# Kernel optimization log

Measured on AMD Instinct MI355X. Metric: run time of the kernel, lower is better.

Reference implementation:

```python
import jax, jax.numpy as jnp
import numpy as np

HEADS = 4
DIM_HEAD = 32
SCALE = 10.0  # scale=10 init arg
HIDDEN = HEADS * DIM_HEAD


def _l2norm(t, eps=1e-12):
    # matches torch F.normalize(t, dim=-1): normalize over last axis (flattened spatial)
    n = jnp.sqrt(jnp.sum(t * t, axis=-1, keepdims=True))
    return t / jnp.maximum(n, eps)


def setup_inputs() -> dict:
    key = jax.random.key(0)
    k1, k2, k3, k4, k5 = jax.random.split(key, 5)
    b, dim, H, W = 2, 128, 64, 64
    x = jax.random.normal(k1, (b, dim, H, W), jnp.float32)
    y = jax.random.normal(k2, (b, dim, H, W), jnp.float32)
    # to_qkv: Conv2d(dim, 3*hidden, 1, bias=False) -> weight (3*hidden, dim)
    w_qkv = jax.random.normal(k3, (3 * HIDDEN, dim), jnp.float32) / np.sqrt(dim)
    # to_out: Conv2d(hidden, dim, 1) -> weight (dim, hidden) + bias (dim,)
    w_out = jax.random.normal(k4, (dim, HIDDEN), jnp.float32) / np.sqrt(HIDDEN)
    b_out = jax.random.normal(k5, (dim,), jnp.float32) * 0.01
    return {"x": x, "y": y, "w_qkv": w_qkv, "w_out": w_out, "b_out": b_out}


def reference(x, y, w_qkv, w_out, b_out):
    b, c, H, W = x.shape
    n_x = H * W
    n_y = y.shape[2] * y.shape[3]
    xf = x.reshape(b, c, n_x)
    yf = y.reshape(b, c, n_y)
    # 1x1 conv == channel GEMM
    qkv_x = jnp.einsum('oc,bcn->bon', w_qkv, xf)
    qkv_y = jnp.einsum('oc,bcn->bon', w_qkv, yf)
    # only q from x, k/v from y are used downstream
    q_x = qkv_x[:, :HIDDEN].reshape(b, HEADS, DIM_HEAD, n_x)
    k_y = qkv_y[:, HIDDEN:2 * HIDDEN].reshape(b, HEADS, DIM_HEAD, n_y)
    v_y = qkv_y[:, 2 * HIDDEN:].reshape(b, HEADS, DIM_HEAD, n_y)
    q = _l2norm(q_x)
    k = _l2norm(k_y)
    sim = jnp.einsum('bhdi,bhdj->bhij', q, k) * SCALE  # [b,h,n_x,n_y]
    attn = jax.nn.softmax(sim, axis=-1)
    out = jnp.einsum('bhij,bhdj->bhdi', attn, v_y)  # [b,h,d,n_x]
    out = out.reshape(b, HIDDEN, H, W)  # 'b h (x y) d -> b (h d) x y'
    return jnp.einsum('oc,bcHW->boHW', w_out, out) + b_out[None, :, None, None]
```

## Files before the change

kernel.cpp:

```cpp
#include <hip/hip_runtime.h>
#include <hip/hip_bf16.h>

#define HEADS 4
#define DIMH  32
#define HID   128
#define DIM   128
#define NSP   4096
#define QSCALE_LOG2E 14.426950408889634f

typedef __attribute__((ext_vector_type(4)))  float f32x4;
typedef __attribute__((ext_vector_type(16))) float f32x16;
typedef __attribute__((ext_vector_type(8)))  short s16x8;

__device__ __forceinline__ unsigned cvtpk_bf16(float a, float b) {
  unsigned d;
  asm("v_cvt_pk_bf16_f32 %0, %1, %2" : "=v"(d) : "v"(a), "v"(b));
  return d;
}

__global__ __launch_bounds__(256) void k_cvt(const float* __restrict__ x,
                                             const float* __restrict__ y,
                                             __hip_bfloat16* __restrict__ xt,
                                             __hip_bfloat16* __restrict__ yt) {
  int bid = blockIdx.x;
  int t = bid >> 7, rem = bid & 127;
  int b = rem >> 6, nt = rem & 63;
  int n0 = nt * 64;
  const float* src = (t ? y : x) + (size_t)b * DIM * NSP;
  __hip_bfloat16* dst = (t ? yt : xt) + (size_t)b * NSP * DIM;

  __shared__ alignas(16) __hip_bfloat16 tile[64 * 136];
  int n = threadIdx.x & 63, c0 = threadIdx.x >> 6;
  const float* sp = src + n0 + n;
#pragma unroll
  for (int cc = 0; cc < 32; ++cc) {
    int c = cc * 4 + c0;
    tile[n * 136 + c] = __float2bfloat16(sp[(size_t)c * NSP]);
  }
  __syncthreads();
  int rrow = threadIdx.x >> 2, cb = (threadIdx.x & 3) * 32;
  __hip_bfloat16* op = dst + (size_t)(n0 + rrow) * DIM + cb;
  const __hip_bfloat16* ip = tile + rrow * 136 + cb;
#pragma unroll
  for (int k = 0; k < 4; ++k)
    *(s16x8*)(op + k * 8) = *(const s16x8*)(ip + k * 8);
}

__global__ __launch_bounds__(256, 4) void k_qkvm(const __hip_bfloat16* __restrict__ xt,
                                                 const __hip_bfloat16* __restrict__ yt,
                                                 const float* __restrict__ w,
                                                 float* __restrict__ ssp,
                                                 float* __restrict__ Qf,
                                                 __hip_bfloat16* __restrict__ Kr,
                                                 __hip_bfloat16* __restrict__ Vb) {
  int xcd = blockIdx.x & 7;
  int r = blockIdx.x >> 3;
  int ot = r >> 2;
  int nts = r & 3;
  int tile = xcd * 4 + nts;
  int n0 = tile * 256;
  int lane = threadIdx.x & 63, wave = threadIdx.x >> 6;
  int l31 = lane & 31, hi = lane >> 5;
  int orow = ot * 32 + l31;

  s16x8 wf[8];
  const float* wr = w + orow * DIM + hi * 8;
#pragma unroll
  for (int k = 0; k < 8; ++k) {
    f32x4 a = *(const f32x4*)(wr + k * 16);
    f32x4 b2 = *(const f32x4*)(wr + k * 16 + 4);
    union { unsigned u[4]; s16x8 v; } p;
    p.u[0] = cvtpk_bf16(a[0], a[1]);
    p.u[1] = cvtpk_bf16(a[2], a[3]);
    p.u[2] = cvtpk_bf16(b2[0], b2[1]);
    p.u[3] = cvtpk_bf16(b2[2], b2[3]);
    wf[k] = p.v;
  }

  const __hip_bfloat16* src = (ot < 4 ? xt : yt);
  int nw = n0 + wave * 64;
  f32x16 acc0 = {}, acc1 = {};
#pragma unroll
  for (int k = 0; k < 8; ++k) {
    s16x8 b0 = *(const s16x8*)(src + (size_t)(nw + l31) * DIM + k * 16 + hi * 8);
    s16x8 b1 = *(const s16x8*)(src + (size_t)(nw + 32 + l31) * DIM + k * 16 + hi * 8);
    acc0 = __builtin_amdgcn_mfma_f32_32x32x16_bf16(wf[k], b0, acc0, 0, 0, 0);
    acc1 = __builtin_amdgcn_mfma_f32_32x32x16_bf16(wf[k], b1, acc1, 0, 0, 0);
  }

  int b = nw >> 12;
  if (ot < 8) {
    int h = ot & 3;
    if (ot < 4) {
#pragma unroll
      for (int nt = 0; nt < 2; ++nt) {
        int np = (nw + nt * 32 + l31) & 4095;
        float* base = Qf + ((size_t)((b * HEADS + h) * NSP + np)) * DIMH;
        const f32x16& A = nt ? acc1 : acc0;
#pragma unroll
        for (int m = 0; m < 4; ++m) {
          f32x4 v = { A[4 * m], A[4 * m + 1], A[4 * m + 2], A[4 * m + 3] };
          *(f32x4*)(base + 8 * m + 4 * hi) = v;
        }
      }
    } else {
#pragma unroll
      for (int nt = 0; nt < 2; ++nt) {
        int np = (nw + nt * 32 + l31) & 4095;
        __hip_bfloat16* base = Kr + ((size_t)((b * HEADS + h) * NSP + np)) * DIMH;
        const f32x16& A = nt ? acc1 : acc0;
#pragma unroll
        for (int m = 0; m < 4; ++m) {
          uint2 p2;
          p2.x = cvtpk_bf16(A[4 * m], A[4 * m + 1]);
          p2.y = cvtpk_bf16(A[4 * m + 2], A[4 * m + 3]);
          *(uint2*)(base + 8 * m + 4 * hi) = p2;
        }
      }
    }
    float p[16];
#pragma unroll
    for (int r2 = 0; r2 < 16; ++r2) p[r2] = acc0[r2] * acc0[r2] + acc1[r2] * acc1[r2];
#pragma unroll
    for (int r2 = 0; r2 < 16; ++r2) {
#pragma unroll
      for (int m2 = 1; m2 < 32; m2 <<= 1) p[r2] += __shfl_xor(p[r2], m2);
    }
    if (l31 == 0) {
      int t = (ot < 4 ? 0 : 1);
      int widx = (tile & 15) * 4 + wave;
      int rbase = (t * 2 + b) * 128 + h * 32;
#pragma unroll
      for (int r2 = 0; r2 < 16; ++r2) {
        int row = (r2 & 3) + 8 * (r2 >> 2) + 4 * hi;
        ssp[(size_t)(rbase + row) * 64 + widx] = p[r2];
      }
    }
  } else {
    int h = ot - 8;
#pragma unroll
    for (int nt = 0; nt < 2; ++nt) {
      int np = (nw + nt * 32 + l31) & 4095;
      const f32x16& A = nt ? acc1 : acc0;
#pragma unroll
      for (int r2 = 0; r2 < 16; ++r2) {
        int d = (r2 & 3) + 8 * (r2 >> 2) + 4 * hi;
        Vb[((size_t)((b * HEADS + h) * DIMH + d)) * NSP + np] = __float2bfloat16(A[r2]);
      }
    }
  }
}

__global__ __launch_bounds__(512) void k_fac(const float* __restrict__ ssp,
                                             float* __restrict__ fsc) {
  int bh = blockIdx.x;
  int b = bh >> 2, h = bh & 3;
  int tid = threadIdx.x;
  int qk = tid >> 8, d = (tid >> 3) & 31, jj = tid & 7;
  const float* pp = ssp + (size_t)((qk * 2 + b) * 128 + h * 32 + d) * 64 + jj * 8;
  float s = 0.f;
#pragma unroll
  for (int k = 0; k < 8; ++k) s += pp[k];
  s += __shfl_down(s, 1); s += __shfl_down(s, 2); s += __shfl_down(s, 4);
  __shared__ float red[2][32];
  if (jj == 0) red[qk][d] = s;
  __syncthreads();
  if (tid < 32) {
    float vq = 1.f / fmaxf(sqrtf(red[0][tid]), 0.1f);
    float vk = 1.f / fmaxf(sqrtf(red[1][tid]), 0.1f);
    fsc[bh * 32 + tid] = vq * vk * QSCALE_LOG2E;
  }
}

__device__ __forceinline__ void glds16(const __hip_bfloat16* g, __hip_bfloat16* l) {
  __builtin_amdgcn_global_load_lds(
      (const __attribute__((address_space(1))) unsigned int*)(const void*)g,
      (__attribute__((address_space(3))) unsigned int*)(void*)l, 16, 0, 0);
}

__device__ __forceinline__ void attn_sub2(const __hip_bfloat16* kbase,
                                          const __hip_bfloat16* vbase,
                                          int s, int l31, int hi,
                                          s16x8 qb0, s16x8 qb1,
                                          f32x16& O, float& lsum) {
  int krx = (l31 + (l31 >> 2)) & 3;
  int vrx = l31 & 7;
  const __hip_bfloat16* krow = kbase + (s * 32 + l31) * DIMH;
  s16x8 kf0 = *(const s16x8*)(krow + (((hi) ^ krx) << 3));
  s16x8 kf1 = *(const s16x8*)(krow + (((2 + hi) ^ krx) << 3));
  f32x16 z = {};
  f32x16 sv = __builtin_amdgcn_mfma_f32_32x32x16_bf16(kf0, qb0, z, 0, 0, 0);
  sv        = __builtin_amdgcn_mfma_f32_32x32x16_bf16(kf1, qb1, sv, 0, 0, 0);
  float p[16];
#pragma unroll
  for (int r = 0; r < 16; ++r) p[r] = __builtin_amdgcn_exp2f(sv[r]);
  float t0 = 0.f, t1 = 0.f;
#pragma unroll
  for (int r = 0; r < 16; r += 2) { t0 += p[r]; t1 += p[r + 1]; }
  lsum += t0 + t1;
  unsigned wA[4], wB[4];
#pragma unroll
  for (int m = 0; m < 4; ++m) {
    wA[m] = cvtpk_bf16(p[4 * m], p[4 * m + 1]);
    wB[m] = cvtpk_bf16(p[4 * m + 2], p[4 * m + 3]);
  }
  const __hip_bfloat16* vrow = vbase + l31 * 64;
#define PV_CHUNK(c2, vfrag)                                                    \
  {                                                                            \
    unsigned a0 = wA[2 * (c2)], a1 = wA[2 * (c2) + 1];                         \
    unsigned b0 = wB[2 * (c2)], b1 = wB[2 * (c2) + 1];                         \
    asm("v_permlane32_swap_b32 %0, %1" : "+v"(a0), "+v"(a1));                  \
    asm("v_permlane32_swap_b32 %0, %1" : "+v"(b0), "+v"(b1));                  \
    union { unsigned u[4]; s16x8 v; } pa;                                      \
    pa.u[0] = a0; pa.u[1] = b0; pa.u[2] = a1; pa.u[3] = b1;                    \
    O = __builtin_amdgcn_mfma_f32_32x32x16_bf16(pa.v, vfrag, O, 0, 0, 0);      \
  }
#pragma unroll
  for (int c2 = 0; c2 < 2; ++c2) {
    int cc = s * 2 + c2;
    s16x8 vf = *(const s16x8*)(vrow + (((cc * 2 + hi) ^ vrx) << 3));
    PV_CHUNK(c2, vf);
  }
#undef PV_CHUNK
}

__global__ __launch_bounds__(1024, 4) void k_attn(const float* __restrict__ Qf,
                                                  const __hip_bfloat16* __restrict__ Kt,
                                                  const __hip_bfloat16* __restrict__ Vb,
                                                  const float* __restrict__ fsc,
                                                  __hip_bfloat16* __restrict__ Otb) {
  int bh = blockIdx.x & 7, qt = blockIdx.x >> 3;
  int tid = threadIdx.x, lane = tid & 63, wave = tid >> 6;
  int qsub = wave & 3, jq = wave >> 2;
  int l31 = lane & 31, hi = lane >> 5;
  int i0 = qt * 128 + qsub * 32;
  int jbase = jq * 1024;

  __shared__ alignas(16) char smem[65536];
  __shared__ float Llds[16][64];
  __hip_bfloat16* KsB = (__hip_bfloat16*)smem;
  __hip_bfloat16* VsB = KsB + 16384;
  float* Olds = (float*)smem;

  const __hip_bfloat16* kg = Kt + (size_t)bh * NSP * DIMH;
  const __hip_bfloat16* vg = Vb + (size_t)bh * DIMH * NSP;

  const float* qpf = Qf + ((size_t)bh * NSP + i0 + l31) * DIMH;
  const float* fb = fsc + bh * 32;
  s16x8 qb0, qb1;
  {
    f32x4 a0 = *(const f32x4*)(qpf + hi * 8);
    f32x4 a1 = *(const f32x4*)(qpf + hi * 8 + 4);
    f32x4 a2 = *(const f32x4*)(qpf + 16 + hi * 8);
    f32x4 a3 = *(const f32x4*)(qpf + 16 + hi * 8 + 4);
    f32x4 f0 = *(const f32x4*)(fb + hi * 8);
    f32x4 f1 = *(const f32x4*)(fb + hi * 8 + 4);
    f32x4 f2 = *(const f32x4*)(fb + 16 + hi * 8);
    f32x4 f3 = *(const f32x4*)(fb + 16 + hi * 8 + 4);
    union { unsigned u[4]; s16x8 v; } p0, p1;
    p0.u[0] = cvtpk_bf16(a0[0] * f0[0], a0[1] * f0[1]);
    p0.u[1] = cvtpk_bf16(a0[2] * f0[2], a0[3] * f0[3]);
    p0.u[2] = cvtpk_bf16(a1[0] * f1[0], a1[1] * f1[1]);
    p0.u[3] = cvtpk_bf16(a1[2] * f1[2], a1[3] * f1[3]);
    p1.u[0] = cvtpk_bf16(a2[0] * f2[0], a2[1] * f2[1]);
    p1.u[1] = cvtpk_bf16(a2[2] * f2[2], a2[3] * f2[3]);
    p1.u[2] = cvtpk_bf16(a3[0] * f3[0], a3[1] * f3[1]);
    p1.u[3] = cvtpk_bf16(a3[2] * f3[2], a3[3] * f3[3]);
    qb0 = p0.v; qb1 = p1.v;
  }

  int ku = qsub * 64 + lane;
  int krow = ku >> 2;
  int kchunk = (ku & 3) ^ ((krow + (krow >> 2)) & 3);
  const __hip_bfloat16* ksrc0 = kg + (size_t)krow * DIMH + (kchunk << 3);
  int vd = ku >> 3;
  int vchunk = (ku & 7) ^ (vd & 7);
  const __hip_bfloat16* vsrc0 = vg + (size_t)vd * NSP + (vchunk << 3);
  int lbase = qsub * 512;

  f32x16 O = {};
  float ls0 = 0.f, ls1 = 0.f;

  glds16(ksrc0 + (size_t)jbase * DIMH, &KsB[(jq * 2 + 0) * 2048 + lbase]);
  glds16(vsrc0 + jbase,                &VsB[(jq * 2 + 0) * 2048 + lbase]);
  asm volatile("s_waitcnt vmcnt(0)" ::: "memory");
  __syncthreads();

#pragma unroll 1
  for (int t = 0; t < 16; ++t) {
    int buf = t & 1;
    if (t < 15) {
      int j1 = jbase + (t + 1) * 64;
      glds16(ksrc0 + (size_t)j1 * DIMH, &KsB[(jq * 2 + (buf ^ 1)) * 2048 + lbase]);
      glds16(vsrc0 + j1,                &VsB[(jq * 2 + (buf ^ 1)) * 2048 + lbase]);
    }
    const __hip_bfloat16* kbase = &KsB[(jq * 2 + buf) * 2048];
    const __hip_bfloat16* vbase = &VsB[(jq * 2 + buf) * 2048];
    attn_sub2(kbase, vbase, 0, l31, hi, qb0, qb1, O, ls0);
    attn_sub2(kbase, vbase, 1, l31, hi, qb0, qb1, O, ls1);
    if (t < 15) {
      asm volatile("s_waitcnt vmcnt(0)" ::: "memory");
      __syncthreads();
    }
  }

  float lsum = ls0 + ls1;
  float lw = lsum + __shfl_xor(lsum, 32);
  Llds[wave][lane] = lw;
  __syncthreads();
  if (jq) {
    float* od = Olds + (size_t)(qsub * 3 + (jq - 1)) * 1088;
#pragma unroll
    for (int r = 0; r < 16; ++r) od[r * 68 + lane] = O[r];
  }
  __syncthreads();
  if (jq == 0) {
    float ltot = lw + Llds[wave + 4][lane] + Llds[wave + 8][lane] + Llds[wave + 12][lane];
    if (hi == 0) Llds[wave][l31] = ltot;
    float* o0 = Olds + (size_t)(qsub * 3) * 1088;
    float* o1 = o0 + 1088;
    float* o2 = o1 + 1088;
#pragma unroll
    for (int r = 0; r < 16; ++r) {
      int i = (r & 3) + 8 * (r >> 2) + 4 * hi;
      float li = Llds[wave][i];
      float sum = O[r] + o0[r * 68 + lane] + o1[r * 68 + lane] + o2[r * 68 + lane];
      o0[r * 68 + lane] = sum / li;
    }
  }
  __syncthreads();
  {
    int q2 = tid >> 8;
    int i  = (tid >> 3) & 31;
    int cp = tid & 7;
    int r  = (i & 3) | ((i >> 3) << 2);
    int h2 = (i >> 2) & 1;
    const float* o0 = Olds + (size_t)(q2 * 3) * 1088 + r * 68 + h2 * 32 + cp * 4;
    uint2 pv;
    pv.x = cvtpk_bf16(o0[0], o0[1]);
    pv.y = cvtpk_bf16(o0[2], o0[3]);
    int b2 = bh >> 2, h = bh & 3;
    __hip_bfloat16* dst = Otb + ((size_t)(b2 * NSP + qt * 128 + q2 * 32 + i)) * HID + h * 32 + cp * 4;
    *(uint2*)dst = pv;
  }
}

__global__ __launch_bounds__(256, 4) void k_projm(const __hip_bfloat16* __restrict__ Otb,
                                                  const float* __restrict__ w,
                                                  const float* __restrict__ bias,
                                                  float* __restrict__ out) {
  int xcd = blockIdx.x & 7;
  int ot  = (blockIdx.x >> 3) & 3;
  int yy  = blockIdx.x >> 5;
  int tile = xcd * 8 + yy;
  int n0 = tile * 128;
  int lane = threadIdx.x & 63, wave = threadIdx.x >> 6;
  int l31 = lane & 31, hi = lane >> 5;
  int orow = ot * 32 + l31;

  s16x8 wf[8];
  const float* wr = w + orow * HID + hi * 8;
#pragma unroll
  for (int k = 0; k < 8; ++k) {
    f32x4 a = *(const f32x4*)(wr + k * 16);
    f32x4 b2 = *(const f32x4*)(wr + k * 16 + 4);
    union { unsigned u[4]; s16x8 v; } p;
    p.u[0] = cvtpk_bf16(a[0], a[1]);
    p.u[1] = cvtpk_bf16(a[2], a[3]);
    p.u[2] = cvtpk_bf16(b2[0], b2[1]);
    p.u[3] = cvtpk_bf16(b2[2], b2[3]);
    wf[k] = p.v;
  }

  int nw = n0 + wave * 32;
  int b = nw >> 12, np = nw & 4095;
  const __hip_bfloat16* src = Otb + ((size_t)(b * NSP + np)) * HID;
  f32x16 acc = {};
#pragma unroll
  for (int k = 0; k < 8; ++k) {
    s16x8 bfr = *(const s16x8*)(src + (size_t)l31 * HID + k * 16 + hi * 8);
    acc = __builtin_amdgcn_mfma_f32_32x32x16_bf16(wf[k], bfr, acc, 0, 0, 0);
  }

  float* outb = out + (size_t)b * DIM * NSP + np + l31;
#pragma unroll
  for (int r2 = 0; r2 < 16; ++r2) {
    int o = ot * 32 + (r2 & 3) + 8 * (r2 >> 2) + 4 * hi;
    outb[(size_t)o * NSP] = acc[r2] + bias[o];
  }
}

extern "C" void kernel_launch(void* const* d_in, const int* in_sizes, int n_in,
                              void* d_out, int out_size, void* d_ws, size_t ws_size,
                              hipStream_t stream) {
  const float* x     = (const float*)d_in[0];
  const float* y     = (const float*)d_in[1];
  const float* w_qkv = (const float*)d_in[2];
  const float* w_out = (const float*)d_in[3];
  const float* b_out = (const float*)d_in[4];
  float* out = (float*)d_out;

  char* ws = (char*)d_ws;
  __hip_bfloat16* xt  = (__hip_bfloat16*)(ws);
  __hip_bfloat16* yt  = (__hip_bfloat16*)(ws + (2  << 20));
  float* Qf           = (float*)(ws + (4  << 20));
  __hip_bfloat16* Kr  = (__hip_bfloat16*)(ws + (8  << 20));
  __hip_bfloat16* Vb  = (__hip_bfloat16*)(ws + (10 << 20));
  __hip_bfloat16* Otb = (__hip_bfloat16*)(ws + (12 << 20));
  float* ssp          = (float*)(ws + (16 << 20));
  float* fsc          = (float*)(ws + (16 << 20) + (128 << 10));

  k_cvt   <<<256,  256,  0, stream>>>(x, y, xt, yt);
  k_qkvm  <<<384,  256,  0, stream>>>(xt, yt, w_qkv, ssp, Qf, Kr, Vb);
  k_fac   <<<8,    512,  0, stream>>>(ssp, fsc);
  k_attn  <<<256,  1024, 0, stream>>>(Qf, Kr, Vb, fsc, Otb);
  k_projm <<<256,  256,  0, stream>>>(Otb, w_out, b_out, out);
}
```

Before: 58.48 us.

## Fuse norm-factor kernel into attention and halve attention block query tile

Removes the separate k_fac launch; each attention block now reduces the partial squared sums itself and computes the q/k scale factors in LDS. Attention blocks shrink from 1024 to 512 threads with 64 queries per block, doubling the grid to 512 blocks, so each wave stages two K/V slices per step. The V swizzle is changed to fold in a higher row bit, meant to reduce LDS bank conflicts. This saves one kernel launch and a global round trip, but every block redundantly recomputes the factors, and K/V traffic per query roughly doubles.

```diff
diff --git a/kernel.cpp b/kernel.cpp
--- a/kernel.cpp
+++ b/kernel.cpp
@@ -151,27 +151,6 @@
   }
 }
 
-__global__ __launch_bounds__(512) void k_fac(const float* __restrict__ ssp,
-                                             float* __restrict__ fsc) {
-  int bh = blockIdx.x;
-  int b = bh >> 2, h = bh & 3;
-  int tid = threadIdx.x;
-  int qk = tid >> 8, d = (tid >> 3) & 31, jj = tid & 7;
-  const float* pp = ssp + (size_t)((qk * 2 + b) * 128 + h * 32 + d) * 64 + jj * 8;
-  float s = 0.f;
-#pragma unroll
-  for (int k = 0; k < 8; ++k) s += pp[k];
-  s += __shfl_down(s, 1); s += __shfl_down(s, 2); s += __shfl_down(s, 4);
-  __shared__ float red[2][32];
-  if (jj == 0) red[qk][d] = s;
-  __syncthreads();
-  if (tid < 32) {
-    float vq = 1.f / fmaxf(sqrtf(red[0][tid]), 0.1f);
-    float vk = 1.f / fmaxf(sqrtf(red[1][tid]), 0.1f);
-    fsc[bh * 32 + tid] = vq * vk * QSCALE_LOG2E;
-  }
-}
-
 __device__ __forceinline__ void glds16(const __hip_bfloat16* g, __hip_bfloat16* l) {
   __builtin_amdgcn_global_load_lds(
       (const __attribute__((address_space(1))) unsigned int*)(const void*)g,
@@ -184,7 +163,7 @@
                                           s16x8 qb0, s16x8 qb1,
                                           f32x16& O, float& lsum) {
   int krx = (l31 + (l31 >> 2)) & 3;
-  int vrx = l31 & 7;
+  int vrx = (l31 + (l31 >> 3)) & 7;
   const __hip_bfloat16* krow = kbase + (s * 32 + l31) * DIMH;
   s16x8 kf0 = *(const s16x8*)(krow + (((hi) ^ krx) << 3));
   s16x8 kf1 = *(const s16x8*)(krow + (((2 + hi) ^ krx) << 3));
@@ -224,39 +203,61 @@
 #undef PV_CHUNK
 }
 
-__global__ __launch_bounds__(1024, 4) void k_attn(const float* __restrict__ Qf,
-                                                  const __hip_bfloat16* __restrict__ Kt,
-                                                  const __hip_bfloat16* __restrict__ Vb,
-                                                  const float* __restrict__ fsc,
-                                                  __hip_bfloat16* __restrict__ Otb) {
+__global__ __launch_bounds__(512, 4) void k_attn(const float* __restrict__ Qf,
+                                                 const __hip_bfloat16* __restrict__ Kt,
+                                                 const __hip_bfloat16* __restrict__ Vb,
+                                                 const float* __restrict__ ssp,
+                                                 __hip_bfloat16* __restrict__ Otb) {
   int bh = blockIdx.x & 7, qt = blockIdx.x >> 3;
   int tid = threadIdx.x, lane = tid & 63, wave = tid >> 6;
-  int qsub = wave & 3, jq = wave >> 2;
+  int qsub = wave & 1, jq = wave >> 1;
   int l31 = lane & 31, hi = lane >> 5;
-  int i0 = qt * 128 + qsub * 32;
+  int i0 = qt * 64 + qsub * 32;
   int jbase = jq * 1024;
+  int b = bh >> 2, h = bh & 3;
 
   __shared__ alignas(16) char smem[65536];
-  __shared__ float Llds[16][64];
+  __shared__ float Llds[8][64];
+  __shared__ float redl[64];
+  __shared__ float fscl[32];
   __hip_bfloat16* KsB = (__hip_bfloat16*)smem;
   __hip_bfloat16* VsB = KsB + 16384;
   float* Olds = (float*)smem;
 
+  {
+    int row = tid >> 3, part = tid & 7;
+    int qk = row >> 5, r32 = row & 31;
+    const float* pp = ssp + (size_t)((qk * 2 + b) * 128 + h * 32 + r32) * 64 + part * 8;
+    float s = 0.f;
+#pragma unroll
+    for (int k = 0; k < 8; ++k) s += pp[k];
+    s += __shfl_xor(s, 1);
+    s += __shfl_xor(s, 2);
+    s += __shfl_xor(s, 4);
+    if (part == 0) redl[row] = s;
+  }
+  __syncthreads();
+  if (tid < 32) {
+    float vq = 1.f / fmaxf(sqrtf(redl[tid]), 0.1f);
+    float vk = 1.f / fmaxf(sqrtf(redl[tid + 32]), 0.1f);
+    fscl[tid] = vq * vk * QSCALE_LOG2E;
+  }
+  __syncthreads();
+
   const __hip_bfloat16* kg = Kt + (size_t)bh * NSP * DIMH;
   const __hip_bfloat16* vg = Vb + (size_t)bh * DIMH * NSP;
 
   const float* qpf = Qf + ((size_t)bh * NSP + i0 + l31) * DIMH;
-  const float* fb = fsc + bh * 32;
   s16x8 qb0, qb1;
   {
     f32x4 a0 = *(const f32x4*)(qpf + hi * 8);
     f32x4 a1 = *(const f32x4*)(qpf + hi * 8 + 4);
     f32x4 a2 = *(const f32x4*)(qpf + 16 + hi * 8);
     f32x4 a3 = *(const f32x4*)(qpf + 16 + hi * 8 + 4);
-    f32x4 f0 = *(const f32x4*)(fb + hi * 8);
-    f32x4 f1 = *(const f32x4*)(fb + hi * 8 + 4);
-    f32x4 f2 = *(const f32x4*)(fb + 16 + hi * 8);
-    f32x4 f3 = *(const f32x4*)(fb + 16 + hi * 8 + 4);
+    f32x4 f0 = *(const f32x4*)(fscl + hi * 8);
+    f32x4 f1 = *(const f32x4*)(fscl + hi * 8 + 4);
+    f32x4 f2 = *(const f32x4*)(fscl + 16 + hi * 8);
+    f32x4 f3 = *(const f32x4*)(fscl + 16 + hi * 8 + 4);
     union { unsigned u[4]; s16x8 v; } p0, p1;
     p0.u[0] = cvtpk_bf16(a0[0] * f0[0], a0[1] * f0[1]);
     p0.u[1] = cvtpk_bf16(a0[2] * f0[2], a0[3] * f0[3]);
@@ -271,31 +272,38 @@
 
   int ku = qsub * 64 + lane;
   int krow = ku >> 2;
-  int kchunk = (ku & 3) ^ ((krow + (krow >> 2)) & 3);
-  const __hip_bfloat16* ksrc0 = kg + (size_t)krow * DIMH + (kchunk << 3);
-  int vd = ku >> 3;
-  int vchunk = (ku & 7) ^ (vd & 7);
-  const __hip_bfloat16* vsrc0 = vg + (size_t)vd * NSP + (vchunk << 3);
-  int lbase = qsub * 512;
+  int kch = (ku & 3) ^ ((krow + (krow >> 2)) & 3);
+  const __hip_bfloat16* ksrc0 = kg + (size_t)krow * DIMH + (kch << 3);
+  int vdA = ku >> 3;
+  int vchA = (ku & 7) ^ ((vdA + (vdA >> 3)) & 7);
+  const __hip_bfloat16* vsrcA = vg + (size_t)vdA * NSP + (vchA << 3);
+  int vdB = vdA + 16;
+  int vchB = (ku & 7) ^ ((vdB + (vdB >> 3)) & 7);
+  const __hip_bfloat16* vsrcB = vg + (size_t)vdB * NSP + (vchB << 3);
 
   f32x16 O = {};
   float ls0 = 0.f, ls1 = 0.f;
 
-  glds16(ksrc0 + (size_t)jbase * DIMH, &KsB[(jq * 2 + 0) * 2048 + lbase]);
-  glds16(vsrc0 + jbase,                &VsB[(jq * 2 + 0) * 2048 + lbase]);
+#define STAGE(j0, buf)                                                         \
+  {                                                                            \
+    __hip_bfloat16* kd = KsB + (jq * 2 + (buf)) * 2048;                        \
+    __hip_bfloat16* vd = VsB + (jq * 2 + (buf)) * 2048;                        \
+    glds16(ksrc0 + (size_t)(j0) * DIMH,      kd + qsub * 512);                 \
+    glds16(ksrc0 + (size_t)(j0 + 32) * DIMH, kd + 1024 + qsub * 512);          \
+    glds16(vsrcA + (j0), vd + qsub * 512);                                     \
+    glds16(vsrcB + (j0), vd + 1024 + qsub * 512);                              \
+  }
+
+  STAGE(jbase, 0);
   asm volatile("s_waitcnt vmcnt(0)" ::: "memory");
   __syncthreads();
 
 #pragma unroll 1
   for (int t = 0; t < 16; ++t) {
     int buf = t & 1;
-    if (t < 15) {
-      int j1 = jbase + (t + 1) * 64;
-      glds16(ksrc0 + (size_t)j1 * DIMH, &KsB[(jq * 2 + (buf ^ 1)) * 2048 + lbase]);
-      glds16(vsrc0 + j1,                &VsB[(jq * 2 + (buf ^ 1)) * 2048 + lbase]);
-    }
-    const __hip_bfloat16* kbase = &KsB[(jq * 2 + buf) * 2048];
-    const __hip_bfloat16* vbase = &VsB[(jq * 2 + buf) * 2048];
+    if (t < 15) STAGE(jbase + (t + 1) * 64, buf ^ 1);
+    const __hip_bfloat16* kbase = KsB + (jq * 2 + buf) * 2048;
+    const __hip_bfloat16* vbase = VsB + (jq * 2 + buf) * 2048;
     attn_sub2(kbase, vbase, 0, l31, hi, qb0, qb1, O, ls0);
     attn_sub2(kbase, vbase, 1, l31, hi, qb0, qb1, O, ls1);
     if (t < 15) {
@@ -303,6 +311,7 @@
       __syncthreads();
     }
   }
+#undef STAGE
 
   float lsum = ls0 + ls1;
   float lw = lsum + __shfl_xor(lsum, 32);
@@ -315,7 +324,7 @@
   }
   __syncthreads();
   if (jq == 0) {
-    float ltot = lw + Llds[wave + 4][lane] + Llds[wave + 8][lane] + Llds[wave + 12][lane];
+    float ltot = lw + Llds[wave + 2][lane] + Llds[wave + 4][lane] + Llds[wave + 6][lane];
     if (hi == 0) Llds[wave][l31] = ltot;
     float* o0 = Olds + (size_t)(qsub * 3) * 1088;
     float* o1 = o0 + 1088;
@@ -339,8 +348,7 @@
     uint2 pv;
     pv.x = cvtpk_bf16(o0[0], o0[1]);
     pv.y = cvtpk_bf16(o0[2], o0[3]);
-    int b2 = bh >> 2, h = bh & 3;
-    __hip_bfloat16* dst = Otb + ((size_t)(b2 * NSP + qt * 128 + q2 * 32 + i)) * HID + h * 32 + cp * 4;
+    __hip_bfloat16* dst = Otb + ((size_t)(b * NSP + qt * 64 + q2 * 32 + i)) * HID + h * 32 + cp * 4;
     *(uint2*)dst = pv;
   }
 }
@@ -408,11 +416,9 @@
   __hip_bfloat16* Vb  = (__hip_bfloat16*)(ws + (10 << 20));
   __hip_bfloat16* Otb = (__hip_bfloat16*)(ws + (12 << 20));
   float* ssp          = (float*)(ws + (16 << 20));
-  float* fsc          = (float*)(ws + (16 << 20) + (128 << 10));
-
-  k_cvt   <<<256,  256,  0, stream>>>(x, y, xt, yt);
-  k_qkvm  <<<384,  256,  0, stream>>>(xt, yt, w_qkv, ssp, Qf, Kr, Vb);
-  k_fac   <<<8,    512,  0, stream>>>(ssp, fsc);
-  k_attn  <<<256,  1024, 0, stream>>>(Qf, Kr, Vb, fsc, Otb);
-  k_projm <<<256,  256,  0, stream>>>(Otb, w_out, b_out, out);
-}
+
+  k_cvt   <<<256, 256, 0, stream>>>(x, y, xt, yt);
+  k_qkvm  <<<384, 256, 0, stream>>>(xt, yt, w_qkv, ssp, Qf, Kr, Vb);
+  k_attn  <<<512, 512, 0, stream>>>(Qf, Kr, Vb, ssp, Otb);
+  k_projm <<<256, 256, 0, stream>>>(Otb, w_out, b_out, out);
+}
```

New measurement: 57.74 us. Within noise of the previous version (-1.3%).
